# Kernel tuning notes

Hardware: AMD Instinct MI355X
Metric: run time of the kernel (lower is better)

The kernel has to match this reference:

```python
import jax, jax.numpy as jnp
import numpy as np

EMBED_DIM = 1024
NUM_HEADS = 16
HEAD_DIM = EMBED_DIM // NUM_HEADS


def setup_inputs() -> dict:
    key = jax.random.key(0)
    ks = jax.random.split(key, 11)
    N, S, D = 2, 2048, EMBED_DIM
    scale = 1.0 / np.sqrt(D)
    inp = {
        "query": jax.random.normal(ks[0], (N, S, D), jnp.float32),
        "key": jax.random.normal(ks[1], (N, S, D), jnp.float32),
        "value": jax.random.normal(ks[2], (N, S, D), jnp.float32),
        # Dense layer params (kernel [D_in, D_out], bias [D_out])
        "Wq": jax.random.normal(ks[3], (D, D), jnp.float32) * scale,
        "bq": jnp.zeros((D,), jnp.float32),
        "Wk": jax.random.normal(ks[4], (D, D), jnp.float32) * scale,
        "bk": jnp.zeros((D,), jnp.float32),
        "Wv": jax.random.normal(ks[5], (D, D), jnp.float32) * scale,
        "bv": jnp.zeros((D,), jnp.float32),
        "Wp": jax.random.normal(ks[6], (D, D), jnp.float32) * scale,
        "bp": jnp.zeros((D,), jnp.float32),
    }
    return inp


def reference(query, key, value, Wq, bq, Wk, bk, Wv, bv, Wp, bp):
    N, S, D = query.shape
    H, Hd = NUM_HEADS, D // NUM_HEADS
    # Linear projections, then split heads: [N, H, S, Hd]
    def split_heads(x):
        return x.reshape(N, S, H, Hd).transpose(0, 2, 1, 3)
    q = split_heads(query @ Wq + bq)
    k = split_heads(key @ Wk + bk)
    v = split_heads(value @ Wv + bv)
    # Scaled dot-product attention; materializes [N, H, S, S] scores
    e = jnp.einsum("bhsd,bhtd->bhst", q, k) / jnp.sqrt(jnp.asarray(Hd, jnp.float32))
    a = jax.nn.softmax(e, axis=-1)
    # Dropout is identity in inference mode (keras Dropout default)
    out = jnp.einsum("bhst,bhtd->bhsd", a, v)
    out = out.transpose(0, 2, 1, 3).reshape(N, S, D)
    return out @ Wp + bp
```

## Files before the change

kernel.cpp:

```cpp
#include <hip/hip_runtime.h>
#include <cstdint>
#include <cstddef>

typedef _Float16 f16;
typedef f16 f16x2 __attribute__((ext_vector_type(2)));
typedef f16 f16x8 __attribute__((ext_vector_type(8)));
typedef __fp16 hf16x2 __attribute__((ext_vector_type(2)));
typedef float f32x4 __attribute__((ext_vector_type(4)));
typedef float f32x16 __attribute__((ext_vector_type(16)));
typedef unsigned int u32;

#define S_LEN 2048
#define DIM 1024
#define NBATCH 2
#define NHEAD 16
#define HDIM 64
#define M_TOT (NBATCH * S_LEN)

#define QSCALE 0.18033688011112042f

#define OFF_XQ 0ull
#define OFF_XK (OFF_XQ + (size_t)M_TOT * DIM * 2)
#define OFF_XV (OFF_XK + (size_t)M_TOT * DIM * 2)
#define OFF_WT (OFF_XV + (size_t)M_TOT * DIM * 2)
#define OFF_Q  (OFF_WT + 4ull * DIM * DIM * 2)
#define OFF_K  (OFF_Q + (size_t)M_TOT * DIM * 2)
#define OFF_VT (OFF_K + (size_t)M_TOT * DIM * 2)
#define OFF_AO (OFF_VT + (size_t)M_TOT * DIM * 2)

typedef const __attribute__((address_space(1))) void GVp;
typedef __attribute__((address_space(3))) void LVp;
__device__ __forceinline__ void gload16(const void* g, void* l) {
  __builtin_amdgcn_global_load_lds((GVp*)g, (LVp*)l, 16, 0, 0);
}

__device__ __forceinline__ float fast_exp2(float x) {
  float r;
  asm("v_exp_f32 %0, %1" : "=v"(r) : "v"(x));
  return r;
}

__global__ __launch_bounds__(256) void cast_x_kernel(
    const float* __restrict__ q, const float* __restrict__ k, const float* __restrict__ v,
    f16* __restrict__ oq, f16* __restrict__ ok, f16* __restrict__ ov) {
  const float* src = blockIdx.y == 0 ? q : blockIdx.y == 1 ? k : v;
  f16* dst = blockIdx.y == 0 ? oq : blockIdx.y == 1 ? ok : ov;
  size_t i = ((size_t)blockIdx.x * 256 + threadIdx.x) * 8;
  float4 a = *(const float4*)(src + i);
  float4 b = *(const float4*)(src + i + 4);
  f16x8 o;
  o[0] = (f16)a.x; o[1] = (f16)a.y; o[2] = (f16)a.z; o[3] = (f16)a.w;
  o[4] = (f16)b.x; o[5] = (f16)b.y; o[6] = (f16)b.z; o[7] = (f16)b.w;
  *(f16x8*)(dst + i) = o;
}

__global__ __launch_bounds__(256) void transpose_w_kernel(
    const float* __restrict__ Wq, const float* __restrict__ Wk,
    const float* __restrict__ Wv, const float* __restrict__ Wp,
    f16* __restrict__ out) {
  const float* W = blockIdx.z == 0 ? Wq : blockIdx.z == 1 ? Wk : blockIdx.z == 2 ? Wv : Wp;
  f16* Wt = out + (size_t)blockIdx.z * DIM * DIM;
  __shared__ f16 tile[64][72];
  const int kt = blockIdx.x * 64, nt = blockIdx.y * 64;
  const int t = threadIdx.x, r = t >> 2, c0 = (t & 3) * 16;
#pragma unroll
  for (int i = 0; i < 16; i += 4) {
    float4 vv = *(const float4*)(W + (size_t)(kt + r) * DIM + nt + c0 + i);
    tile[r][c0 + i + 0] = (f16)vv.x; tile[r][c0 + i + 1] = (f16)vv.y;
    tile[r][c0 + i + 2] = (f16)vv.z; tile[r][c0 + i + 3] = (f16)vv.w;
  }
  __syncthreads();
  f16x8 o0, o1;
#pragma unroll
  for (int i = 0; i < 8; ++i) { o0[i] = tile[c0 + i][r]; o1[i] = tile[c0 + 8 + i][r]; }
  *(f16x8*)(Wt + (size_t)(nt + r) * DIM + kt + c0) = o0;
  *(f16x8*)(Wt + (size_t)(nt + r) * DIM + kt + c0 + 8) = o1;
}

__device__ __forceinline__ void gemm_core(const f16* __restrict__ A, const f16* __restrict__ B,
                                          char* lds, f32x4 acc[4][4]) {
  const int tid = threadIdx.x;
  const int wid = tid >> 6, lane = tid & 63;
  const int l15 = lane & 15, l4 = lane >> 4;
  const int wm = (wid >> 1) * 64, wn = (wid & 1) * 64;
  const int srow = tid >> 2;
  const int scol = (tid & 3) * 8;
  const f16* gA = A + (size_t)srow * DIM + scol;
  const f16* gB = B + (size_t)srow * DIM + scol;
  const int ldst = wid * 1024;

  gload16(gA,            lds + ldst);
  gload16(gA + 64 * DIM, lds + 4096 + ldst);
  gload16(gB,            lds + 8192 + ldst);
  gload16(gB + 64 * DIM, lds + 12288 + ldst);
  __syncthreads();

  for (int kt = 0; kt < DIM / 32; ++kt) {
    char* cur = lds + (kt & 1) * 16384;
    if (kt + 1 < DIM / 32) {
      char* nxt = lds + ((kt + 1) & 1) * 16384;
      const f16* ga = gA + (kt + 1) * 32;
      const f16* gb = gB + (kt + 1) * 32;
      gload16(ga,            nxt + ldst);
      gload16(ga + 64 * DIM, nxt + 4096 + ldst);
      gload16(gb,            nxt + 8192 + ldst);
      gload16(gb + 64 * DIM, nxt + 12288 + ldst);
    }
    f16x8 af[4], bf[4];
#pragma unroll
    for (int mt = 0; mt < 4; ++mt)
      af[mt] = *(const f16x8*)(cur + (wm + mt * 16 + l15) * 64 + l4 * 16);
#pragma unroll
    for (int nt = 0; nt < 4; ++nt)
      bf[nt] = *(const f16x8*)(cur + 8192 + (wn + nt * 16 + l15) * 64 + l4 * 16);
#pragma unroll
    for (int mt = 0; mt < 4; ++mt)
#pragma unroll
      for (int nt = 0; nt < 4; ++nt)
        acc[mt][nt] = __builtin_amdgcn_mfma_f32_16x16x32_f16(af[mt], bf[nt], acc[mt][nt], 0, 0, 0);
    __syncthreads();
  }
}


__global__ __launch_bounds__(256) void proj_kernel(
    const f16* __restrict__ Xq, const f16* __restrict__ Xk, const f16* __restrict__ Xv,
    const f16* __restrict__ Wt,
    const float* __restrict__ bq, const float* __restrict__ bk, const float* __restrict__ bv,
    f16* __restrict__ Q, f16* __restrict__ Kh, f16* __restrict__ Vt) {
  __shared__ __align__(16) char lds[32768];
  const int m0 = blockIdx.x * 128, n0 = blockIdx.y * 128;
  const int z = blockIdx.z;
  const f16* X = z == 0 ? Xq : z == 1 ? Xk : Xv;
  const f16* W = Wt + (size_t)z * DIM * DIM;
  const float* bias = z == 0 ? bq : z == 1 ? bk : bv;
  f32x4 acc[4][4] = {};
  gemm_core(X + (size_t)m0 * DIM, W + (size_t)n0 * DIM, lds, acc);

  const int tid = threadIdx.x, wid = tid >> 6, lane = tid & 63;
  const int l15 = lane & 15, l4 = lane >> 4;
  const int wm = (wid >> 1) * 64, wn = (wid & 1) * 64;
#pragma unroll
  for (int nt = 0; nt < 4; ++nt) {
    const int col = n0 + wn + nt * 16 + l15;
    const float bb = bias[col];
    const int hh = col >> 6, d = col & 63;
#pragma unroll
    for (int mt = 0; mt < 4; ++mt)
#pragma unroll
      for (int j = 0; j < 4; ++j) {
        const int row = m0 + wm + mt * 16 + l4 * 4 + j;
        const float v = acc[mt][nt][j] + bb;
        const int n = row >> 11, s = row & (S_LEN - 1);
        const size_t panel = (size_t)(n * NHEAD + hh);
        if (z == 0) {
          const size_t a = panel * (S_LEN * HDIM) + (size_t)(s >> 5) * 2048 +
                           (d >> 4) * 512 + ((d >> 3) & 1) * 256 + (s & 31) * 8 + (d & 7);
          Q[a] = (f16)(v * QSCALE);
        } else if (z == 1) {
          const size_t a = panel * (S_LEN * HDIM) + (size_t)(s >> 5) * 2048 +
                           (d >> 4) * 512 + ((d >> 3) & 1) * 256 + (s & 31) * 8 + (d & 7);
          Kh[a] = (f16)v;
        } else {
          const size_t a = panel * (S_LEN * HDIM) + (size_t)(s >> 6) * 4096 +
                           (d >> 5) * 2048 + ((s >> 4) & 3) * 512 + ((s >> 3) & 1) * 256 +
                           (d & 31) * 8 + (s & 7);
          Vt[a] = (f16)v;
        }
      }
  }
}

__global__ __launch_bounds__(256) void outproj_kernel(
    const f16* __restrict__ A, const f16* __restrict__ Wt,
    const float* __restrict__ bias, float* __restrict__ Out) {
  __shared__ __align__(16) char lds[32768];
  const int m0 = blockIdx.x * 128, n0 = blockIdx.y * 128;
  f32x4 acc[4][4] = {};
  gemm_core(A + (size_t)m0 * DIM, Wt + (size_t)n0 * DIM, lds, acc);

  const int tid = threadIdx.x, wid = tid >> 6, lane = tid & 63;
  const int l15 = lane & 15, l4 = lane >> 4;
  const int wm = (wid >> 1) * 64, wn = (wid & 1) * 64;
#pragma unroll
  for (int nt = 0; nt < 4; ++nt) {
    const int col = n0 + wn + nt * 16 + l15;
    const float bb = bias[col];
#pragma unroll
    for (int mt = 0; mt < 4; ++mt)
#pragma unroll
      for (int j = 0; j < 4; ++j) {
        const int row = m0 + wm + mt * 16 + l4 * 4 + j;
        Out[(size_t)row * DIM + col] = acc[mt][nt][j] + bb;
      }
  }
}

__global__ __launch_bounds__(256, 2) void attn_kernel(
    const f16* __restrict__ Q, const f16* __restrict__ K,
    const f16* __restrict__ Vt, f16* __restrict__ AO) {
  const int qt = blockIdx.x, h = blockIdx.y, b = blockIdx.z;
  const int tid = threadIdx.x;
  const int lane = tid & 63, wid = tid >> 6;
  const int l31 = lane & 31, hi = lane >> 5;

  __shared__ __align__(16) char kv_lds[3][16384];

  const int q0 = qt * 128 + wid * 32;
  const size_t panel = (size_t)(b * NHEAD + h) * (S_LEN * HDIM);
  const f16* Qp = Q + panel + (size_t)(q0 >> 5) * 2048;
  const char* KpB = (const char*)(K + panel);
  const char* VpB = (const char*)(Vt + panel);

  f16x8 qf[4];
#pragma unroll
  for (int sk = 0; sk < 4; ++sk)
    qf[sk] = *(const f16x8*)(Qp + sk * 512 + hi * 256 + l31 * 8);

  f32x16 accO[2] = {};
  float lacc0 = 0.f, lacc1 = 0.f, lacc2 = 0.f, lacc3 = 0.f;

  auto STAGE = [&](int it, int buf) {
    const char* gK = KpB + (size_t)it * 8192 + tid * 16;
    const char* gV = VpB + (size_t)it * 8192 + tid * 16;
    char* lb = &kv_lds[buf][wid * 1024];
    gload16(gK,        lb);
    gload16(gK + 4096, lb + 4096);
    gload16(gV,        lb + 8192);
    gload16(gV + 4096, lb + 12288);
  };

  auto QK = [&](int buf, f32x16 (&st)[2]) {
    const char* lk = &kv_lds[buf][0];
    f16x8 kf[2][4];
#pragma unroll
    for (int tt = 0; tt < 2; ++tt)
#pragma unroll
      for (int sk = 0; sk < 4; ++sk)
        kf[tt][sk] = *(const f16x8*)(lk + tt * 4096 + sk * 1024 + lane * 16);
    __builtin_amdgcn_s_setprio(1);
#pragma unroll
    for (int tt = 0; tt < 2; ++tt) {
      st[tt] = (f32x16)(0.f);
#pragma unroll
      for (int sk = 0; sk < 4; ++sk)
        st[tt] = __builtin_amdgcn_mfma_f32_32x32x16_f16(kf[tt][sk], qf[sk], st[tt], 0, 0, 0);
    }
    __builtin_amdgcn_s_setprio(0);
  };

  auto PHASE = [&](f32x16 (&st)[2], int buf) {
    const char* lv = &kv_lds[buf][8192];
    f16x8 vf[2][4];
#pragma unroll
    for (int dt = 0; dt < 2; ++dt)
#pragma unroll
      for (int s = 0; s < 4; ++s)
        vf[dt][s] = *(const f16x8*)(lv + dt * 4096 + s * 1024 + lane * 16);

    u32 pk[2][8];
#pragma unroll
    for (int tt = 0; tt < 2; ++tt)
#pragma unroll
      for (int j = 0; j < 8; ++j) {
        const float p0 = fast_exp2(st[tt][2 * j]);
        const float p1 = fast_exp2(st[tt][2 * j + 1]);
        const float ps = p0 + p1;
        if (((tt * 8 + j) & 3) == 0) lacc0 += ps;
        else if (((tt * 8 + j) & 3) == 1) lacc1 += ps;
        else if (((tt * 8 + j) & 3) == 2) lacc2 += ps;
        else lacc3 += ps;
        union { hf16x2 h; u32 w; } cv;
        cv.h = __builtin_amdgcn_cvt_pkrtz(p0, p1);
        pk[tt][j] = cv.w;
      }

    __builtin_amdgcn_s_setprio(1);
#pragma unroll
    for (int s = 0; s < 4; ++s) {
      const int tt = s >> 1, sl = s & 1;
      u32 w0 = pk[tt][4 * sl + 0], w2 = pk[tt][4 * sl + 2];
      u32 w1 = pk[tt][4 * sl + 1], w3 = pk[tt][4 * sl + 3];
      asm("v_permlane32_swap_b32 %0, %1" : "+v"(w0), "+v"(w2));
      asm("v_permlane32_swap_b32 %0, %1" : "+v"(w1), "+v"(w3));
      union { u32 w[4]; f16x8 v; } pf;
      pf.w[0] = w0; pf.w[1] = w1; pf.w[2] = w2; pf.w[3] = w3;
      accO[0] = __builtin_amdgcn_mfma_f32_32x32x16_f16(vf[0][s], pf.v, accO[0], 0, 0, 0);
      accO[1] = __builtin_amdgcn_mfma_f32_32x32x16_f16(vf[1][s], pf.v, accO[1], 0, 0, 0);
    }
    __builtin_amdgcn_s_setprio(0);
  };

  const int NIT = S_LEN / 64;

  STAGE(0, 0);
  STAGE(1, 1);

  f32x16 st[2];
  int bcur = 0;
  for (int it = 0; it < NIT - 1; ++it) {
    asm volatile("s_waitcnt vmcnt(4)" ::: "memory");
    __builtin_amdgcn_sched_barrier(0);
    __builtin_amdgcn_s_barrier();
    __builtin_amdgcn_sched_barrier(0);
    if (it + 2 < NIT) {
      int bn = bcur + 2; if (bn >= 3) bn -= 3;
      STAGE(it + 2, bn);
    }
    QK(bcur, st);
    PHASE(st, bcur);
    if (++bcur >= 3) bcur = 0;
  }
  asm volatile("s_waitcnt vmcnt(0)" ::: "memory");
  __builtin_amdgcn_sched_barrier(0);
  __builtin_amdgcn_s_barrier();
  __builtin_amdgcn_sched_barrier(0);
  QK(bcur, st);
  PHASE(st, bcur);

  const float l_loc = (lacc0 + lacc1) + (lacc2 + lacc3);
  const float l_all = l_loc + __shfl_xor(l_loc, 32);
  const float inv = 1.f / l_all;
  f16* aop = AO + ((size_t)(b * S_LEN + q0 + l31)) * DIM + h * HDIM;
#pragma unroll
  for (int dt = 0; dt < 2; ++dt)
#pragma unroll
    for (int j = 0; j < 8; ++j) {
      union { f16x2 h; u32 w; } cv;
      cv.h[0] = (f16)(accO[dt][2 * j] * inv);
      cv.h[1] = (f16)(accO[dt][2 * j + 1] * inv);
      const int d = ((2 * j) & 3) + 8 * ((2 * j) >> 2) + 4 * hi + dt * 32;
      *(f16x2*)(aop + d) = cv.h;
    }
}

extern "C" void kernel_launch(void* const* d_in, const int* in_sizes, int n_in,
                              void* d_out, int out_size, void* d_ws, size_t ws_size,
                              hipStream_t stream) {
  (void)in_sizes; (void)n_in; (void)out_size; (void)ws_size;
  const float* q  = (const float*)d_in[0];
  const float* k  = (const float*)d_in[1];
  const float* v  = (const float*)d_in[2];
  const float* Wq = (const float*)d_in[3];
  const float* bq = (const float*)d_in[4];
  const float* Wk = (const float*)d_in[5];
  const float* bk = (const float*)d_in[6];
  const float* Wv = (const float*)d_in[7];
  const float* bv = (const float*)d_in[8];
  const float* Wp = (const float*)d_in[9];
  const float* bp = (const float*)d_in[10];

  char* ws = (char*)d_ws;
  f16* Xq  = (f16*)(ws + OFF_XQ);
  f16* Xk  = (f16*)(ws + OFF_XK);
  f16* Xv  = (f16*)(ws + OFF_XV);
  f16* Wt  = (f16*)(ws + OFF_WT);
  f16* Qs  = (f16*)(ws + OFF_Q);
  f16* Kh  = (f16*)(ws + OFF_K);
  f16* Vts = (f16*)(ws + OFF_VT);
  f16* AO  = (f16*)(ws + OFF_AO);

  cast_x_kernel<<<dim3(2048, 3, 1), 256, 0, stream>>>(q, k, v, Xq, Xk, Xv);
  transpose_w_kernel<<<dim3(16, 16, 4), 256, 0, stream>>>(Wq, Wk, Wv, Wp, Wt);
  proj_kernel<<<dim3(32, 8, 3), 256, 0, stream>>>(Xq, Xk, Xv, Wt, bq, bk, bv, Qs, Kh, Vts);
  attn_kernel<<<dim3(16, 16, 2), 256, 0, stream>>>(Qs, Kh, Vts, AO);
  outproj_kernel<<<dim3(32, 8, 1), 256, 0, stream>>>(AO, Wt + 3ull * DIM * DIM, bp, (float*)d_out);
}
```

Measured before the change: 132.0 us.

## Software-pipeline attention loop so QK of next tile overlaps exp/PV of current

Restructures the attention main loop into a two-stage software pipeline: the QK^T MFMAs for tile i+1 are issued while the exp/pack and PV MFMAs for tile i run, using ping-pong score registers unrolled by two. The intent is to hide the exp/VALU latency behind matrix-core work. The sync now waits for vmcnt(0) instead of vmcnt(4), which may expose more global-load latency. The extra live registers for two score sets and the K fragments may also raise register pressure.

```diff
diff --git a/kernel.cpp b/kernel.cpp
--- a/kernel.cpp
+++ b/kernel.cpp
@@ -39,6 +39,14 @@
   asm("v_exp_f32 %0, %1" : "=v"(r) : "v"(x));
   return r;
 }
+
+#define SYNC()                                               \
+  do {                                                       \
+    asm volatile("s_waitcnt vmcnt(0)" ::: "memory");         \
+    __builtin_amdgcn_sched_barrier(0);                       \
+    __builtin_amdgcn_s_barrier();                            \
+    __builtin_amdgcn_sched_barrier(0);                       \
+  } while (0)
 
 __global__ __launch_bounds__(256) void cast_x_kernel(
     const float* __restrict__ q, const float* __restrict__ k, const float* __restrict__ v,
@@ -230,14 +238,24 @@
     gload16(gV + 4096, lb + 12288);
   };
 
-  auto QK = [&](int buf, f32x16 (&st)[2]) {
+  auto READK = [&](int buf, f16x8 (&kf)[2][4]) {
     const char* lk = &kv_lds[buf][0];
-    f16x8 kf[2][4];
 #pragma unroll
     for (int tt = 0; tt < 2; ++tt)
 #pragma unroll
       for (int sk = 0; sk < 4; ++sk)
         kf[tt][sk] = *(const f16x8*)(lk + tt * 4096 + sk * 1024 + lane * 16);
+  };
+  auto READV = [&](int buf, f16x8 (&vf)[2][4]) {
+    const char* lv = &kv_lds[buf][8192];
+#pragma unroll
+    for (int dt = 0; dt < 2; ++dt)
+#pragma unroll
+      for (int s = 0; s < 4; ++s)
+        vf[dt][s] = *(const f16x8*)(lv + dt * 4096 + s * 1024 + lane * 16);
+  };
+
+  auto QKc = [&](const f16x8 (&kf)[2][4], f32x16 (&st)[2]) {
     __builtin_amdgcn_s_setprio(1);
 #pragma unroll
     for (int tt = 0; tt < 2; ++tt) {
@@ -249,16 +267,7 @@
     __builtin_amdgcn_s_setprio(0);
   };
 
-  auto PHASE = [&](f32x16 (&st)[2], int buf) {
-    const char* lv = &kv_lds[buf][8192];
-    f16x8 vf[2][4];
-#pragma unroll
-    for (int dt = 0; dt < 2; ++dt)
-#pragma unroll
-      for (int s = 0; s < 4; ++s)
-        vf[dt][s] = *(const f16x8*)(lv + dt * 4096 + s * 1024 + lane * 16);
-
-    u32 pk[2][8];
+  auto EXPPACK = [&](const f32x16 (&st)[2], u32 (&pk)[2][8]) {
 #pragma unroll
     for (int tt = 0; tt < 2; ++tt)
 #pragma unroll
@@ -274,7 +283,9 @@
         cv.h = __builtin_amdgcn_cvt_pkrtz(p0, p1);
         pk[tt][j] = cv.w;
       }
-
+  };
+
+  auto PVc = [&](u32 (&pk)[2][8], const f16x8 (&vf)[2][4]) {
     __builtin_amdgcn_s_setprio(1);
 #pragma unroll
     for (int s = 0; s < 4; ++s) {
@@ -293,30 +304,53 @@
 
   const int NIT = S_LEN / 64;
 
+  f16x8 kf[2][4], vf[2][4];
+  f32x16 stA[2], stB[2];
+  u32 pk[2][8];
+
   STAGE(0, 0);
   STAGE(1, 1);
-
-  f32x16 st[2];
-  int bcur = 0;
-  for (int it = 0; it < NIT - 1; ++it) {
-    asm volatile("s_waitcnt vmcnt(4)" ::: "memory");
-    __builtin_amdgcn_sched_barrier(0);
-    __builtin_amdgcn_s_barrier();
-    __builtin_amdgcn_sched_barrier(0);
-    if (it + 2 < NIT) {
-      int bn = bcur + 2; if (bn >= 3) bn -= 3;
-      STAGE(it + 2, bn);
-    }
-    QK(bcur, st);
-    PHASE(st, bcur);
-    if (++bcur >= 3) bcur = 0;
-  }
-  asm volatile("s_waitcnt vmcnt(0)" ::: "memory");
-  __builtin_amdgcn_sched_barrier(0);
+  SYNC();
+  READK(0, kf);
+  QKc(kf, stA);
+
+  int b_cur = 0;
+  for (int it = 0; it < NIT - 2; it += 2) {
+    SYNC();
+    int bs = b_cur + 2; if (bs >= 3) bs -= 3;
+    STAGE(it + 2, bs);
+    int bn = b_cur + 1; if (bn >= 3) bn -= 3;
+    READK(bn, kf);
+    EXPPACK(stA, pk);
+    QKc(kf, stB);
+    READV(b_cur, vf);
+    PVc(pk, vf);
+    b_cur = bn;
+    SYNC();
+    bs = b_cur + 2; if (bs >= 3) bs -= 3;
+    STAGE(it + 3, bs);
+    bn = b_cur + 1; if (bn >= 3) bn -= 3;
+    READK(bn, kf);
+    EXPPACK(stB, pk);
+    QKc(kf, stA);
+    READV(b_cur, vf);
+    PVc(pk, vf);
+    b_cur = bn;
+  }
+  SYNC();
+  {
+    int bn = b_cur + 1; if (bn >= 3) bn -= 3;
+    READK(bn, kf);
+    EXPPACK(stA, pk);
+    QKc(kf, stB);
+    READV(b_cur, vf);
+    PVc(pk, vf);
+    b_cur = bn;
+  }
   __builtin_amdgcn_s_barrier();
-  __builtin_amdgcn_sched_barrier(0);
-  QK(bcur, st);
-  PHASE(st, bcur);
+  EXPPACK(stB, pk);
+  READV(b_cur, vf);
+  PVc(pk, vf);
 
   const float l_loc = (lacc0 + lacc1) + (lacc2 + lacc3);
   const float l_all = l_loc + __shfl_xor(l_loc, 32);
```

Measured after the change: 131.0 us. No clear change (-0.7%).
